# Optimization experiments

Measured on AMD Instinct MI355X. Metric: run time of the kernel, lower is better.

## Reference

```python
import jax, jax.numpy as jnp
import numpy as np

B, N, C = 64, 1024, 128
H1, H2 = 256, 128
ACTION = N


def _xavier(key, shape):
    lim = float(np.sqrt(6.0 / (shape[0] + shape[1])))
    return jax.random.uniform(key, shape, jnp.float32, -lim, lim)


def setup_inputs() -> dict:
    key = jax.random.key(0)
    ks = jax.random.split(key, 16)
    node_features = jax.random.normal(ks[0], (B, N, 3), jnp.float32)
    adjacency_matrix = jax.random.randint(ks[1], (B, N, N), 0, 2).astype(jnp.int32)
    return {
        "node_features": node_features,
        "adjacency_matrix": adjacency_matrix,
        "W_in": _xavier(ks[2], (3, C)),
        "a_src": _xavier(ks[3], (C, 1)),
        "a_dst": _xavier(ks[4], (C, 1)),
        "a_src2": _xavier(ks[5], (C, 1)),
        "a_dst2": _xavier(ks[6], (C, 1)),
        "W1": _xavier(ks[7], (C, H1)),
        "b1": jnp.zeros((H1,), jnp.float32),
        "W2": _xavier(ks[8], (H1, H2)),
        "b2": jnp.zeros((H2,), jnp.float32),
        "Wpi": _xavier(ks[9], (H2, ACTION)),
        "bpi": jnp.zeros((ACTION,), jnp.float32),
        "Wv": _xavier(ks[10], (H2, 1)),
        "bv": jnp.zeros((1,), jnp.float32),
    }


def _gat_layer(x, mask, a_src, a_dst):
    # x: [B,N,C]; mask: [B,N,N] bool
    ai = jnp.squeeze(x @ a_src, -1)  # [B,N] score of node as source (i)
    aj = jnp.squeeze(x @ a_dst, -1)  # [B,N] score of node as dest (j)
    e = ai[:, :, None] + aj[:, None, :]  # [B,N,N]
    e = jnp.where(e > 0, e, 0.2 * e)  # leaky_relu(0.2)
    e = jnp.where(mask, e, jnp.float32(-1e9))  # masked_fill(-inf)
    alpha = jax.nn.softmax(e, axis=-1)  # [B,N,N]
    out = jnp.einsum("bij,bjc->bic", alpha, x)  # weighted neighbor aggregation
    return jax.nn.relu(out)


def reference(node_features, adjacency_matrix, W_in, a_src, a_dst, a_src2, a_dst2,
              W1, b1, W2, b2, Wpi, bpi, Wv, bv):
    mask = adjacency_matrix > 0
    x = node_features @ W_in  # [B,N,C], no bias
    x = _gat_layer(x, mask, a_src, a_dst)
    x = _gat_layer(x, mask, a_src2, a_dst2)
    x = jnp.mean(x, axis=1)  # [B,C]
    x = jax.nn.relu(x @ W1 + b1)
    x = jax.nn.relu(x @ W2 + b2)
    pi = jax.nn.softmax(x @ Wpi + bpi, axis=1)
    v = x @ Wv + bv
    return (pi, v)
```

## Files before the change

### kernel.cpp

```cpp
#include <hip/hip_runtime.h>

#define Bn 64
#define Nn 1024
#define Cc 128

typedef _Float16 h8 __attribute__((ext_vector_type(8)));
typedef float f4v __attribute__((ext_vector_type(4)));
typedef unsigned long long u64;

__global__ __launch_bounds__(256) void k_feat(
    const float* __restrict__ nf, const float* __restrict__ Win,
    const float* __restrict__ asrc, const float* __restrict__ adst,
    _Float16* __restrict__ X0, float* __restrict__ ai, float* __restrict__ aj,
    float* __restrict__ E, float* __restrict__ G, float* __restrict__ F, float* __restrict__ H) {
  int g = blockIdx.x; int b = g >> 7; int n0 = (g & 127) << 3;
  int t = threadIdx.x; int c = t >> 1; int h = t & 1;
  float w0 = Win[c], w1 = Win[Cc + c], w2 = Win[2 * Cc + c];
  float as_ = asrc[c], ad = adst[c];
  float ps[4], pd[4];
  _Float16 hv[4];
  #pragma unroll
  for (int r = 0; r < 4; r++) {
    int n = n0 + (h << 2) + r;
    const float* p = nf + ((size_t)(b << 10) + n) * 3;
    float x = p[0] * w0 + p[1] * w1 + p[2] * w2;
    hv[r] = (_Float16)x; ps[r] = x * as_; pd[r] = x * ad;
  }
  *(uint2*)(X0 + ((size_t)b << 17) + ((size_t)(g & 127) << 10) + (c << 3) + (h << 2)) = *(uint2*)hv;
  #pragma unroll
  for (int off = 32; off > 1; off >>= 1) {
    #pragma unroll
    for (int r = 0; r < 4; r++) { ps[r] += __shfl_down(ps[r], off, 64); pd[r] += __shfl_down(pd[r], off, 64); }
  }
  __shared__ float red[4][2][4][2];
  int lane = t & 63, wv = t >> 6;
  if (lane < 2) {
    #pragma unroll
    for (int r = 0; r < 4; r++) { red[wv][lane][r][0] = ps[r]; red[wv][lane][r][1] = pd[r]; }
  }
  __syncthreads();
  if (t < 8) {
    int hh = t >> 2, r = t & 3;
    float sa = 0.f, sd = 0.f;
    #pragma unroll
    for (int w = 0; w < 4; w++) { sa += red[w][hh][r][0]; sd += red[w][hh][r][1]; }
    int gi = (b << 10) + n0 + t;
    ai[gi] = sa; aj[gi] = sd;
    E[gi] = __expf(sa); G[gi] = __expf(0.2f * sa);
    F[gi] = __expf(sd); H[gi] = __expf(0.2f * sd);
  }
}

__global__ __launch_bounds__(256) void k_scores2(
    const _Float16* __restrict__ X1,
    const float* __restrict__ asrc, const float* __restrict__ adst,
    float* __restrict__ ai, float* __restrict__ aj,
    float* __restrict__ E, float* __restrict__ G, float* __restrict__ F, float* __restrict__ H) {
  int g = blockIdx.x; int b = g >> 7; int n0 = (g & 127) << 3;
  int t = threadIdx.x; int c = t >> 1; int h = t & 1;
  float as_ = asrc[c], ad = adst[c];
  uint2 raw = *(const uint2*)(X1 + ((size_t)b << 17) + ((size_t)(g & 127) << 10) + (c << 3) + (h << 2));
  const _Float16* hp = (const _Float16*)&raw;
  float ps[4], pd[4];
  #pragma unroll
  for (int r = 0; r < 4; r++) { float x = (float)hp[r]; ps[r] = x * as_; pd[r] = x * ad; }
  #pragma unroll
  for (int off = 32; off > 1; off >>= 1) {
    #pragma unroll
    for (int r = 0; r < 4; r++) { ps[r] += __shfl_down(ps[r], off, 64); pd[r] += __shfl_down(pd[r], off, 64); }
  }
  __shared__ float red[4][2][4][2];
  int lane = t & 63, wv = t >> 6;
  if (lane < 2) {
    #pragma unroll
    for (int r = 0; r < 4; r++) { red[wv][lane][r][0] = ps[r]; red[wv][lane][r][1] = pd[r]; }
  }
  __syncthreads();
  if (t < 8) {
    int hh = t >> 2, r = t & 3;
    float sa = 0.f, sd = 0.f;
    #pragma unroll
    for (int w = 0; w < 4; w++) { sa += red[w][hh][r][0]; sd += red[w][hh][r][1]; }
    int gi = (b << 10) + n0 + t;
    ai[gi] = sa; aj[gi] = sd;
    E[gi] = __expf(sa); G[gi] = __expf(0.2f * sa);
    F[gi] = __expf(sd); H[gi] = __expf(0.2f * sd);
  }
}

template <int LAYER>
__global__ __launch_bounds__(256, 4) void k_agg(
    const _Float16* __restrict__ X, const int* __restrict__ adj,
    const float* __restrict__ ai, const float* __restrict__ E, const float* __restrict__ G,
    const float* __restrict__ aj, const float* __restrict__ F, const float* __restrict__ H,
    u64* __restrict__ pm, _Float16* __restrict__ Y, float* __restrict__ xmp) {
  __shared__ __align__(16) char smem[34304];
  _Float16* sB = (_Float16*)smem;
  _Float16* sA = (_Float16*)(smem + 8192);
  float* s_aj = (float*)(smem + 12288);
  float* s_F  = (float*)(smem + 16384);
  float* s_H  = (float*)(smem + 20480);
  unsigned char* s_pm = (unsigned char*)(smem + 24576);
  float* tile = (float*)smem;

  const int b = blockIdx.y, i0 = blockIdx.x << 6;
  const int tid = threadIdx.x;
  const int lane = tid & 63, wv = tid >> 6;
  const int m = lane & 15, quad = lane >> 4;
  const int wi = wv >> 1, wc = wv & 1;
  const int gbase = b << 10;

  ((float4*)s_aj)[tid] = ((const float4*)(aj + gbase))[tid];
  ((float4*)s_F)[tid]  = ((const float4*)(F + gbase))[tid];
  ((float4*)s_H)[tid]  = ((const float4*)(H + gbase))[tid];

  if (LAYER == 1) {
    ushort* pmu = (ushort*)pm;
    #pragma unroll 2
    for (int pass = 0; pass < 16; ++pass) {
      int r = (wv << 4) + pass;
      const uint4* arow = (const uint4*)(adj + ((size_t)(gbase + i0 + r) << 10));
      uint4 v0 = arow[(lane << 2) | 0], v1 = arow[(lane << 2) | 1];
      uint4 v2 = arow[(lane << 2) | 2], v3 = arow[(lane << 2) | 3];
      unsigned int bits =
          (v0.x) | (v0.y << 1) | (v0.z << 2) | (v0.w << 3) |
          (v1.x << 4) | (v1.y << 5) | (v1.z << 6) | (v1.w << 7) |
          (v2.x << 8) | (v2.y << 9) | (v2.z << 10) | (v2.w << 11) |
          (v3.x << 12) | (v3.y << 13) | (v3.z << 14) | (v3.w << 15);
      *(ushort*)(s_pm + r * 152 + (lane << 1)) = (ushort)bits;
      pmu[((size_t)(gbase + i0 + r) << 6) + lane] = (ushort)bits;
    }
  } else {
    const u64* pmg = pm + (((size_t)(gbase + i0)) << 4);
    #pragma unroll
    for (int k = tid; k < 1024; k += 256) {
      int r = k >> 4, w = k & 15;
      *(u64*)(s_pm + r * 152 + (w << 3)) = pmg[k];
    }
  }

  const int gi = gbase + i0 + lane;
  const float ai_i = ai[gi];
  const float Ed = E[gi], Gd = G[gi];
  float dsum = 0.f;

  f4v acc[2][4];
  #pragma unroll
  for (int a = 0; a < 2; a++)
    #pragma unroll
    for (int ct = 0; ct < 4; ct++) { f4v z = {0.f, 0.f, 0.f, 0.f}; acc[a][ct] = z; }

  const char* xb = (const char*)(X + ((size_t)b << 17));
  __syncthreads();

  for (int kt = 0; kt < 32; ++kt) {
    const int jt = kt << 5;
    const char* gsrc = xb + (jt << 8) + (wv << 11) + lane * 16;
    uint4 r0 = *(const uint4*)gsrc;
    uint4 r1 = *(const uint4*)(gsrc + 1024);
    h8 af;
    {
      const int j0 = jt + (wv << 3);
      float aw[8], fw[8], hw[8];
      *(float4*)&aw[0] = *(const float4*)&s_aj[j0]; *(float4*)&aw[4] = *(const float4*)&s_aj[j0 + 4];
      *(float4*)&fw[0] = *(const float4*)&s_F[j0];  *(float4*)&fw[4] = *(const float4*)&s_F[j0 + 4];
      *(float4*)&hw[0] = *(const float4*)&s_H[j0];  *(float4*)&hw[4] = *(const float4*)&s_H[j0 + 4];
      unsigned int mbyte = s_pm[lane * 152 + (jt >> 3) + wv];
      #pragma unroll
      for (int jj = 0; jj < 8; jj++) {
        float e = ai_i + aw[jj];
        bool pos = e > 0.f;
        float wi_ = pos ? Ed : Gd;
        float wj_ = pos ? fw[jj] : hw[jj];
        float val = ((mbyte >> jj) & 1u) ? wi_ * wj_ : 0.f;
        dsum += val;
        af[jj] = (_Float16)val;
      }
    }
    __syncthreads();
    {
      char* ldst = (char*)sB + (wv << 11) + lane * 16;
      *(uint4*)ldst = r0;
      *(uint4*)(ldst + 1024) = r1;
      *((h8*)sA + (wv << 6) + lane) = af;
    }
    __syncthreads();
    {
      const h8* pA = (const h8*)sA;
      const h8* pB = (const h8*)sB;
      h8 a0 = pA[(quad << 6) + (wi << 5) + m];
      h8 a1 = pA[(quad << 6) + (wi << 5) + 16 + m];
      #pragma unroll
      for (int ct = 0; ct < 4; ct++) {
        h8 bf = pB[(quad << 7) + (wc << 6) + (ct << 4) + m];
        acc[0][ct] = __builtin_amdgcn_mfma_f32_16x16x32_f16(a0, bf, acc[0][ct], 0, 0, 0);
        acc[1][ct] = __builtin_amdgcn_mfma_f32_16x16x32_f16(a1, bf, acc[1][ct], 0, 0, 0);
      }
    }
  }
  __syncthreads();
  float* dsum_s = (float*)(smem + 12288);
  dsum_s[(lane << 2) + wv] = dsum;
  __syncthreads();
  float rd8[2][4];
  #pragma unroll
  for (int a = 0; a < 2; a++)
    #pragma unroll
    for (int r = 0; r < 4; r++) {
      int lr = (wi << 5) + (a << 4) + (quad << 2) + r;
      float4 d4 = *(const float4*)&dsum_s[lr << 2];
      rd8[a][r] = 1.0f / ((d4.x + d4.y) + (d4.z + d4.w));
    }
  __syncthreads();
  #pragma unroll
  for (int a = 0; a < 2; a++)
    #pragma unroll
    for (int ct = 0; ct < 4; ct++)
      #pragma unroll
      for (int r = 0; r < 4; r++) {
        int lr = (wi << 5) + (a << 4) + (quad << 2) + r;
        int c = (wc << 6) + (ct << 4) + m;
        tile[lr * 132 + c] = fmaxf(acc[a][ct][r] * rd8[a][r], 0.f);
      }
  __syncthreads();
  if (LAYER == 1) {
    _Float16 hv[32];
    #pragma unroll
    for (int s = 0; s < 32; s++) {
      int q = (tid << 5) + s;
      int li = ((q >> 10) << 3) + (q & 7), c = (q >> 3) & 127;
      hv[s] = (_Float16)tile[li * 132 + c];
    }
    uint4* o = (uint4*)(Y + ((size_t)b << 17) + ((size_t)i0 << 7) + (tid << 5));
    o[0] = *(uint4*)&hv[0]; o[1] = *(uint4*)&hv[8];
    o[2] = *(uint4*)&hv[16]; o[3] = *(uint4*)&hv[24];
  } else {
    if (tid < 128) {
      float s = 0.f;
      #pragma unroll
      for (int i = 0; i < 64; i++) s += tile[i * 132 + tid];
      xmp[(((b << 4) + blockIdx.x) << 7) + tid] = s;
    }
  }
}

__global__ __launch_bounds__(256) void k_head(
    const float* __restrict__ xmp, const float* __restrict__ W1, const float* __restrict__ b1,
    const float* __restrict__ W2, const float* __restrict__ b2,
    const float* __restrict__ Wpi, const float* __restrict__ bpi,
    const float* __restrict__ Wv, const float* __restrict__ bv,
    float* __restrict__ out) {
  int b = blockIdx.x, t = threadIdx.x;
  __shared__ float xs[128], h1[256], h2[128], red[4];
  if (t < 128) {
    const float* p = xmp + ((size_t)b << 11);
    float s = 0.f;
    #pragma unroll
    for (int xb = 0; xb < 16; xb++) s += p[(xb << 7) + t];
    xs[t] = s * (1.f / 1024.f);
  }
  __syncthreads();
  float s = 0.f;
  #pragma unroll 8
  for (int k = 0; k < 128; k++) s += xs[k] * W1[k * 256 + t];
  h1[t] = fmaxf(s + b1[t], 0.f);
  __syncthreads();
  if (t < 128) {
    float s2 = 0.f;
    #pragma unroll 8
    for (int k = 0; k < 256; k++) s2 += h1[k] * W2[k * 128 + t];
    h2[t] = fmaxf(s2 + b2[t], 0.f);
  }
  __syncthreads();
  float lg[4];
  #pragma unroll
  for (int q = 0; q < 4; q++) {
    int o = t + (q << 8);
    float s3 = 0.f;
    #pragma unroll 8
    for (int k = 0; k < 128; k++) s3 += h2[k] * Wpi[k * 1024 + o];
    lg[q] = s3 + bpi[o];
  }
  float mx = fmaxf(fmaxf(lg[0], lg[1]), fmaxf(lg[2], lg[3]));
  #pragma unroll
  for (int off = 32; off > 0; off >>= 1) mx = fmaxf(mx, __shfl_down(mx, off, 64));
  if ((t & 63) == 0) red[t >> 6] = mx;
  __syncthreads();
  mx = fmaxf(fmaxf(red[0], red[1]), fmaxf(red[2], red[3]));
  __syncthreads();
  float ex[4]; float sum = 0.f;
  #pragma unroll
  for (int q = 0; q < 4; q++) { ex[q] = __expf(lg[q] - mx); sum += ex[q]; }
  #pragma unroll
  for (int off = 32; off > 0; off >>= 1) sum += __shfl_down(sum, off, 64);
  if ((t & 63) == 0) red[t >> 6] = sum;
  __syncthreads();
  sum = red[0] + red[1] + red[2] + red[3];
  float rs = 1.0f / sum;
  #pragma unroll
  for (int q = 0; q < 4; q++) out[((size_t)b << 10) + t + (q << 8)] = ex[q] * rs;
  __syncthreads();
  float vp = (t < 128) ? h2[t] * Wv[t] : 0.f;
  #pragma unroll
  for (int off = 32; off > 0; off >>= 1) vp += __shfl_down(vp, off, 64);
  if ((t & 63) == 0) red[t >> 6] = vp;
  __syncthreads();
  if (t == 0) out[65536 + b] = red[0] + red[1] + red[2] + red[3] + bv[0];
}

extern "C" void kernel_launch(void* const* d_in, const int* in_sizes, int n_in,
                              void* d_out, int out_size, void* d_ws, size_t ws_size,
                              hipStream_t stream) {
  const float* nf    = (const float*)d_in[0];
  const int*   adj   = (const int*)  d_in[1];
  const float* Win   = (const float*)d_in[2];
  const float* asrc  = (const float*)d_in[3];
  const float* adst  = (const float*)d_in[4];
  const float* asrc2 = (const float*)d_in[5];
  const float* adst2 = (const float*)d_in[6];
  const float* W1    = (const float*)d_in[7];
  const float* b1    = (const float*)d_in[8];
  const float* W2    = (const float*)d_in[9];
  const float* b2    = (const float*)d_in[10];
  const float* Wpi   = (const float*)d_in[11];
  const float* bpi   = (const float*)d_in[12];
  const float* Wv    = (const float*)d_in[13];
  const float* bv    = (const float*)d_in[14];
  float* out = (float*)d_out;

  char* ws = (char*)d_ws;
  _Float16* x0 = (_Float16*)(ws);
  _Float16* x1 = (_Float16*)(ws + 16777216);
  u64* pm = (u64*)(ws + 33554432);
  char* S = ws + 41943040;
  float* ai1 = (float*)(S + 0 * 262144);
  float* aj1 = (float*)(S + 1 * 262144);
  float* E1  = (float*)(S + 2 * 262144);
  float* G1  = (float*)(S + 3 * 262144);
  float* F1  = (float*)(S + 4 * 262144);
  float* H1  = (float*)(S + 5 * 262144);
  float* ai2 = (float*)(S + 6 * 262144);
  float* aj2 = (float*)(S + 7 * 262144);
  float* E2  = (float*)(S + 8 * 262144);
  float* G2  = (float*)(S + 9 * 262144);
  float* F2  = (float*)(S + 10 * 262144);
  float* H2  = (float*)(S + 11 * 262144);
  float* xmp = (float*)(S + 12 * 262144);

  k_feat<<<8192, 256, 0, stream>>>(nf, Win, asrc, adst, x0, ai1, aj1, E1, G1, F1, H1);
  dim3 ag(16, Bn);
  k_agg<1><<<ag, 256, 0, stream>>>(x0, adj, ai1, E1, G1, aj1, F1, H1, pm, x1, nullptr);
  k_scores2<<<8192, 256, 0, stream>>>(x1, asrc2, adst2, ai2, aj2, E2, G2, F2, H2);
  k_agg<2><<<ag, 256, 0, stream>>>(x1, nullptr, ai2, E2, G2, aj2, F2, H2, pm, nullptr, xmp);
  k_head<<<Bn, 256, 0, stream>>>(xmp, W1, b1, W2, b2, Wpi, bpi, Wv, bv, out);
}
```

Baseline: 546.3 us.

## Give each wave its own 16 rows and load B fragments directly from global

Restructures the aggregation kernel so each wave owns 16 query rows and all 128 output channels. The attention weights are computed in-register as the MFMA A operand, and the B fragments (X) are read straight from global memory in MFMA layout. This removes the per-iteration LDS staging and the two block barriers in the main loop. The row-sum normalisation and the column reduction now use wave shuffles instead of an LDS tile, which shrinks shared memory. The trade-offs are more redundant global/L2 reads of X (each wave loads the full tile), higher register pressure (launch bounds lowered to 3 blocks), and reliance on the X layout matching the fragment order.

```diff
diff --git a/kernel.cpp b/kernel.cpp
--- a/kernel.cpp
+++ b/kernel.cpp
@@ -89,25 +89,22 @@
 }
 
 template <int LAYER>
-__global__ __launch_bounds__(256, 4) void k_agg(
+__global__ __launch_bounds__(256, 3) void k_agg(
     const _Float16* __restrict__ X, const int* __restrict__ adj,
     const float* __restrict__ ai, const float* __restrict__ E, const float* __restrict__ G,
     const float* __restrict__ aj, const float* __restrict__ F, const float* __restrict__ H,
     u64* __restrict__ pm, _Float16* __restrict__ Y, float* __restrict__ xmp) {
-  __shared__ __align__(16) char smem[34304];
-  _Float16* sB = (_Float16*)smem;
-  _Float16* sA = (_Float16*)(smem + 8192);
-  float* s_aj = (float*)(smem + 12288);
-  float* s_F  = (float*)(smem + 16384);
-  float* s_H  = (float*)(smem + 20480);
-  unsigned char* s_pm = (unsigned char*)(smem + 24576);
-  float* tile = (float*)smem;
+  __shared__ __align__(16) char smem[24064];
+  float* s_aj = (float*)smem;
+  float* s_F  = (float*)(smem + 4096);
+  float* s_H  = (float*)(smem + 8192);
+  unsigned char* s_pm = (unsigned char*)(smem + 12288);
+  float* s_col = (float*)(smem + 22016);
 
   const int b = blockIdx.y, i0 = blockIdx.x << 6;
   const int tid = threadIdx.x;
-  const int lane = tid & 63, wv = tid >> 6;
+  const int lane = tid & 63, w = tid >> 6;
   const int m = lane & 15, quad = lane >> 4;
-  const int wi = wv >> 1, wc = wv & 1;
   const int gbase = b << 10;
 
   ((float4*)s_aj)[tid] = ((const float4*)(aj + gbase))[tid];
@@ -118,7 +115,7 @@
     ushort* pmu = (ushort*)pm;
     #pragma unroll 2
     for (int pass = 0; pass < 16; ++pass) {
-      int r = (wv << 4) + pass;
+      int r = (w << 4) + pass;
       const uint4* arow = (const uint4*)(adj + ((size_t)(gbase + i0 + r) << 10));
       uint4 v0 = arow[(lane << 2) | 0], v1 = arow[(lane << 2) | 1];
       uint4 v2 = arow[(lane << 2) | 2], v3 = arow[(lane << 2) | 3];
@@ -134,111 +131,85 @@
     const u64* pmg = pm + (((size_t)(gbase + i0)) << 4);
     #pragma unroll
     for (int k = tid; k < 1024; k += 256) {
-      int r = k >> 4, w = k & 15;
-      *(u64*)(s_pm + r * 152 + (w << 3)) = pmg[k];
-    }
-  }
-
-  const int gi = gbase + i0 + lane;
+      int r = k >> 4, wd = k & 15;
+      *(u64*)(s_pm + r * 152 + (wd << 3)) = pmg[k];
+    }
+  }
+
+  const int irow = (w << 4) + m;
+  const int gi = gbase + i0 + irow;
   const float ai_i = ai[gi];
   const float Ed = E[gi], Gd = G[gi];
   float dsum = 0.f;
 
-  f4v acc[2][4];
-  #pragma unroll
-  for (int a = 0; a < 2; a++)
-    #pragma unroll
-    for (int ct = 0; ct < 4; ct++) { f4v z = {0.f, 0.f, 0.f, 0.f}; acc[a][ct] = z; }
-
-  const char* xb = (const char*)(X + ((size_t)b << 17));
+  f4v acc[8];
+  #pragma unroll
+  for (int ct = 0; ct < 8; ct++) { f4v z = {0.f, 0.f, 0.f, 0.f}; acc[ct] = z; }
+
+  const h8* xb = (const h8*)(X + ((size_t)b << 17));
+  const int prow = irow * 152;
   __syncthreads();
 
   for (int kt = 0; kt < 32; ++kt) {
-    const int jt = kt << 5;
-    const char* gsrc = xb + (jt << 8) + (wv << 11) + lane * 16;
-    uint4 r0 = *(const uint4*)gsrc;
-    uint4 r1 = *(const uint4*)(gsrc + 1024);
+    const h8* bsrc = xb + (kt << 9) + (quad << 7) + m;
+    h8 bf0 = bsrc[0],  bf1 = bsrc[16], bf2 = bsrc[32],  bf3 = bsrc[48];
+    h8 bf4 = bsrc[64], bf5 = bsrc[80], bf6 = bsrc[96],  bf7 = bsrc[112];
+    const int j0 = (kt << 5) + (quad << 3);
+    float aw[8], fw[8], hw[8];
+    *(float4*)&aw[0] = *(const float4*)&s_aj[j0]; *(float4*)&aw[4] = *(const float4*)&s_aj[j0 + 4];
+    *(float4*)&fw[0] = *(const float4*)&s_F[j0];  *(float4*)&fw[4] = *(const float4*)&s_F[j0 + 4];
+    *(float4*)&hw[0] = *(const float4*)&s_H[j0];  *(float4*)&hw[4] = *(const float4*)&s_H[j0 + 4];
+    unsigned int mb = s_pm[prow + (kt << 2) + quad];
     h8 af;
-    {
-      const int j0 = jt + (wv << 3);
-      float aw[8], fw[8], hw[8];
-      *(float4*)&aw[0] = *(const float4*)&s_aj[j0]; *(float4*)&aw[4] = *(const float4*)&s_aj[j0 + 4];
-      *(float4*)&fw[0] = *(const float4*)&s_F[j0];  *(float4*)&fw[4] = *(const float4*)&s_F[j0 + 4];
-      *(float4*)&hw[0] = *(const float4*)&s_H[j0];  *(float4*)&hw[4] = *(const float4*)&s_H[j0 + 4];
-      unsigned int mbyte = s_pm[lane * 152 + (jt >> 3) + wv];
+    #pragma unroll
+    for (int jj = 0; jj < 8; jj++) {
+      float e = ai_i + aw[jj];
+      bool pos = e > 0.f;
+      float wi_ = pos ? Ed : Gd;
+      float wj_ = pos ? fw[jj] : hw[jj];
+      float val = ((mb >> jj) & 1u) ? wi_ * wj_ : 0.f;
+      dsum += val;
+      af[jj] = (_Float16)val;
+    }
+    acc[0] = __builtin_amdgcn_mfma_f32_16x16x32_f16(af, bf0, acc[0], 0, 0, 0);
+    acc[1] = __builtin_amdgcn_mfma_f32_16x16x32_f16(af, bf1, acc[1], 0, 0, 0);
+    acc[2] = __builtin_amdgcn_mfma_f32_16x16x32_f16(af, bf2, acc[2], 0, 0, 0);
+    acc[3] = __builtin_amdgcn_mfma_f32_16x16x32_f16(af, bf3, acc[3], 0, 0, 0);
+    acc[4] = __builtin_amdgcn_mfma_f32_16x16x32_f16(af, bf4, acc[4], 0, 0, 0);
+    acc[5] = __builtin_amdgcn_mfma_f32_16x16x32_f16(af, bf5, acc[5], 0, 0, 0);
+    acc[6] = __builtin_amdgcn_mfma_f32_16x16x32_f16(af, bf6, acc[6], 0, 0, 0);
+    acc[7] = __builtin_amdgcn_mfma_f32_16x16x32_f16(af, bf7, acc[7], 0, 0, 0);
+  }
+
+  dsum += __shfl_xor(dsum, 16, 64);
+  dsum += __shfl_xor(dsum, 32, 64);
+  float rd[4];
+  #pragma unroll
+  for (int r = 0; r < 4; r++) rd[r] = 1.0f / __shfl(dsum, (quad << 2) + r, 64);
+
+  if (LAYER == 1) {
+    const int g8 = ((i0 + (w << 4)) >> 3) + (quad >> 1);
+    _Float16* yb = Y + ((size_t)b << 17) + (size_t)g8 * 1024 + ((quad & 1) << 2);
+    #pragma unroll
+    for (int ct = 0; ct < 8; ct++) {
+      int c = (ct << 4) + m;
+      _Float16 hv[4];
       #pragma unroll
-      for (int jj = 0; jj < 8; jj++) {
-        float e = ai_i + aw[jj];
-        bool pos = e > 0.f;
-        float wi_ = pos ? Ed : Gd;
-        float wj_ = pos ? fw[jj] : hw[jj];
-        float val = ((mbyte >> jj) & 1u) ? wi_ * wj_ : 0.f;
-        dsum += val;
-        af[jj] = (_Float16)val;
-      }
+      for (int r = 0; r < 4; r++) hv[r] = (_Float16)fmaxf(acc[ct][r] * rd[r], 0.f);
+      *(uint2*)(yb + c * 8) = *(uint2*)hv;
+    }
+  } else {
+    #pragma unroll
+    for (int ct = 0; ct < 8; ct++) {
+      float cs = (fmaxf(acc[ct][0] * rd[0], 0.f) + fmaxf(acc[ct][1] * rd[1], 0.f))
+               + (fmaxf(acc[ct][2] * rd[2], 0.f) + fmaxf(acc[ct][3] * rd[3], 0.f));
+      cs += __shfl_xor(cs, 16, 64);
+      cs += __shfl_xor(cs, 32, 64);
+      if (quad == 0) s_col[(w << 7) + (ct << 4) + m] = cs;
     }
     __syncthreads();
-    {
-      char* ldst = (char*)sB + (wv << 11) + lane * 16;
-      *(uint4*)ldst = r0;
-      *(uint4*)(ldst + 1024) = r1;
-      *((h8*)sA + (wv << 6) + lane) = af;
-    }
-    __syncthreads();
-    {
-      const h8* pA = (const h8*)sA;
-      const h8* pB = (const h8*)sB;
-      h8 a0 = pA[(quad << 6) + (wi << 5) + m];
-      h8 a1 = pA[(quad << 6) + (wi << 5) + 16 + m];
-      #pragma unroll
-      for (int ct = 0; ct < 4; ct++) {
-        h8 bf = pB[(quad << 7) + (wc << 6) + (ct << 4) + m];
-        acc[0][ct] = __builtin_amdgcn_mfma_f32_16x16x32_f16(a0, bf, acc[0][ct], 0, 0, 0);
-        acc[1][ct] = __builtin_amdgcn_mfma_f32_16x16x32_f16(a1, bf, acc[1][ct], 0, 0, 0);
-      }
-    }
-  }
-  __syncthreads();
-  float* dsum_s = (float*)(smem + 12288);
-  dsum_s[(lane << 2) + wv] = dsum;
-  __syncthreads();
-  float rd8[2][4];
-  #pragma unroll
-  for (int a = 0; a < 2; a++)
-    #pragma unroll
-    for (int r = 0; r < 4; r++) {
-      int lr = (wi << 5) + (a << 4) + (quad << 2) + r;
-      float4 d4 = *(const float4*)&dsum_s[lr << 2];
-      rd8[a][r] = 1.0f / ((d4.x + d4.y) + (d4.z + d4.w));
-    }
-  __syncthreads();
-  #pragma unroll
-  for (int a = 0; a < 2; a++)
-    #pragma unroll
-    for (int ct = 0; ct < 4; ct++)
-      #pragma unroll
-      for (int r = 0; r < 4; r++) {
-        int lr = (wi << 5) + (a << 4) + (quad << 2) + r;
-        int c = (wc << 6) + (ct << 4) + m;
-        tile[lr * 132 + c] = fmaxf(acc[a][ct][r] * rd8[a][r], 0.f);
-      }
-  __syncthreads();
-  if (LAYER == 1) {
-    _Float16 hv[32];
-    #pragma unroll
-    for (int s = 0; s < 32; s++) {
-      int q = (tid << 5) + s;
-      int li = ((q >> 10) << 3) + (q & 7), c = (q >> 3) & 127;
-      hv[s] = (_Float16)tile[li * 132 + c];
-    }
-    uint4* o = (uint4*)(Y + ((size_t)b << 17) + ((size_t)i0 << 7) + (tid << 5));
-    o[0] = *(uint4*)&hv[0]; o[1] = *(uint4*)&hv[8];
-    o[2] = *(uint4*)&hv[16]; o[3] = *(uint4*)&hv[24];
-  } else {
     if (tid < 128) {
-      float s = 0.f;
-      #pragma unroll
-      for (int i = 0; i < 64; i++) s += tile[i * 132 + tid];
+      float s = s_col[tid] + s_col[128 + tid] + s_col[256 + tid] + s_col[384 + tid];
       xmp[(((b << 4) + blockIdx.x) << 7) + tid] = s;
     }
   }
```

Result: slower. 564.9 us (+3.4%).
